# Kernel optimization log

Measured on AMD Instinct MI355X. Metric: run time of the kernel, lower is better.

## Reference

```python
import jax, jax.numpy as jnp
import numpy as np

D_MODEL = 1024
N_HEADS = 16
D_HEAD = D_MODEL // N_HEADS
SCALE = 1.0 / float(np.sqrt(D_HEAD))


def setup_inputs() -> dict:
    key = jax.random.key(0)
    ks = jax.random.split(key, 6)
    B, T = 4, 2048
    x = jax.random.normal(ks[0], (B, T, D_MODEL), dtype=jnp.float32)
    # torch Linear weights are [out, in]; y = x @ W.T
    s = 1.0 / np.sqrt(D_MODEL)
    Wq = jax.random.uniform(ks[1], (D_MODEL, D_MODEL), jnp.float32, -s, s)
    Wk = jax.random.uniform(ks[2], (D_MODEL, D_MODEL), jnp.float32, -s, s)
    Wv = jax.random.uniform(ks[3], (D_MODEL, D_MODEL), jnp.float32, -s, s)
    Wo = jax.random.uniform(ks[4], (D_MODEL, D_MODEL), jnp.float32, -s, s)
    bo = jax.random.uniform(ks[5], (D_MODEL,), jnp.float32, -s, s)
    return {"x": x, "Wq": Wq, "Wk": Wk, "Wv": Wv, "Wo": Wo, "bo": bo}


def reference(x, Wq, Wk, Wv, Wo, bo):
    B, T, D = x.shape
    # QKV projections (torch Linear: x @ W.T), split into heads -> [B, H, T, d]
    def heads(y):
        return y.reshape(B, T, N_HEADS, D_HEAD).transpose(0, 2, 1, 3)
    q = heads(x @ Wq.T)
    k = heads(x @ Wk.T)
    v = heads(x @ Wv.T)
    scores = jnp.einsum("bhqd,bhkd->bhqk", q, k) * SCALE  # [B,H,T,T]
    probs = jax.nn.softmax(scores, axis=-1)
    # dropout is identity in eval/inference mode
    out = jnp.einsum("bhqk,bhkd->bhqd", probs, v)  # [B,H,T,d]
    out = out.transpose(0, 2, 1, 3).reshape(B, T, D)
    return out @ Wo.T + bo
```

## Files before the change

### kernel.cpp

```cpp
#include <hip/hip_runtime.h>
#include <stdint.h>

#define D_MODEL 1024
#define NH 16
#define DH 64
#define TSEQ 2048
#define BATCH 4
#define MTOT (BATCH*TSEQ)
#define NQ (MTOT*D_MODEL)
#define WSZ (D_MODEL*D_MODEL)
#define QSCALE 0.18033688f

typedef __attribute__((ext_vector_type(8))) short bf16x8;
typedef __attribute__((ext_vector_type(8))) unsigned short u16x8;
typedef __attribute__((ext_vector_type(4))) float f32x4;
typedef __attribute__((ext_vector_type(2))) float f32x2;
typedef unsigned short u16;
typedef unsigned int u32;

__device__ __forceinline__ void gl_lds16(const void* g, void* l) {
  __builtin_amdgcn_global_load_lds(
      (__attribute__((address_space(1))) void*)g,
      (__attribute__((address_space(3))) void*)l, 16, 0, 0);
}
__device__ __forceinline__ u16 f2bf(float f) {
  u32 u = __builtin_bit_cast(u32, f);
  u = u + 0x7fffu + ((u >> 16) & 1u);
  return (u16)(u >> 16);
}
__device__ __forceinline__ float bf2f(u16 b) {
  u32 u = ((u32)b) << 16;
  return __builtin_bit_cast(float, u);
}
__device__ __forceinline__ u32 pack2bf(float fb, float fa) {
  const u32 ua = __builtin_bit_cast(u32, fa) + 0x8000u;
  const u32 ub = __builtin_bit_cast(u32, fb) + 0x8000u;
  return __builtin_amdgcn_perm(ua, ub, 0x07060302u);
}

__global__ __launch_bounds__(256) void detect_dtype(
    const u32* __restrict__ wq_raw, int* __restrict__ flag)
{
  __shared__ int cnt;
  if (threadIdx.x == 0) cnt = 0;
  __syncthreads();
  int c = 0;
  for (int i = threadIdx.x; i < 2048; i += 256) {
    const u32 e = (wq_raw[i] >> 7) & 0xFFu;
    if (e >= 90u && e <= 126u) ++c;
  }
  atomicAdd(&cnt, c);
  __syncthreads();
  if (threadIdx.x == 0) *flag = (cnt > 1024) ? 1 : 0;
}

__global__ __launch_bounds__(256) void convert_inputs(
    const void* __restrict__ x, const void* __restrict__ wq,
    const void* __restrict__ wk, const void* __restrict__ wv,
    const void* __restrict__ wo,
    u16* __restrict__ xb, u16* __restrict__ wqb, u16* __restrict__ wkb,
    u16* __restrict__ wvb, u16* __restrict__ wob,
    const int* __restrict__ flag_p)
{
  const int flag = *flag_p;
  const int seg = blockIdx.y;
  const void* src; u16* dst; int n;
  switch (seg) {
    case 0:  src = x;  dst = xb;  n = NQ;  break;
    case 1:  src = wq; dst = wqb; n = WSZ; break;
    case 2:  src = wk; dst = wkb; n = WSZ; break;
    case 3:  src = wv; dst = wvb; n = WSZ; break;
    default: src = wo; dst = wob; n = WSZ; break;
  }
  if (flag && seg == 0) return;
  const int idx = (blockIdx.x * 256 + threadIdx.x) * 8;
  if (idx >= n) return;
  if (flag) {
    *(u16x8*)(dst + idx) = *(const u16x8*)((const u16*)src + idx);
  } else {
    const float4 f0 = *(const float4*)((const float*)src + idx);
    const float4 f1 = *(const float4*)((const float*)src + idx + 4);
    union { u16 s[8]; u16x8 v; } u;
    u.s[0] = f2bf(f0.x); u.s[1] = f2bf(f0.y); u.s[2] = f2bf(f0.z); u.s[3] = f2bf(f0.w);
    u.s[4] = f2bf(f1.x); u.s[5] = f2bf(f1.y); u.s[6] = f2bf(f1.z); u.s[7] = f2bf(f1.w);
    *(u16x8*)(dst + idx) = u.v;
  }
}

__global__ __launch_bounds__(256) void qkv_gemm(
    const int* __restrict__ flag_p, const u16* __restrict__ x_raw,
    u16* __restrict__ dout,
    const u16* __restrict__ Wq, const u16* __restrict__ Wk,
    const u16* __restrict__ Wv,
    u16* __restrict__ Ko, u16* __restrict__ VTo)
{
  __shared__ __align__(16) u16 As[2 * 128 * 32];
  __shared__ __align__(16) u16 Bs[2 * 128 * 32];
  const int flag = *flag_p;
  const u16* __restrict__ X = flag ? x_raw : dout;
  u16* __restrict__ QTo = flag ? dout : dout + NQ;
  const int t = threadIdx.x;
  const int z = blockIdx.z;
  const u16* __restrict__ W = (z == 0) ? Wq : (z == 1) ? Wk : Wv;
  const int m0 = blockIdx.x * 128;
  const int n0 = blockIdx.y * 128;
  const int wave = t >> 6, lane = t & 63;
  const int wm = (wave >> 1) * 64, wn = (wave & 1) * 64;
  const int lr = lane & 15, kg = (lane >> 4) * 8;

  const int srow0 = t >> 2, skc = (t & 3) * 8;
  const int srow1 = srow0 + 64;
  const u16* a0 = X + (size_t)(m0 + srow0) * D_MODEL + skc;
  const u16* a1 = X + (size_t)(m0 + srow1) * D_MODEL + skc;
  const u16* b0 = W + (size_t)(n0 + srow0) * D_MODEL + skc;
  const u16* b1 = W + (size_t)(n0 + srow1) * D_MODEL + skc;

  f32x4 acc[4][4] = {};

  for (int kt = 0; kt < D_MODEL / 64; ++kt) {
    gl_lds16(a0,      &As[t * 8]);
    gl_lds16(a1,      &As[(t + 256) * 8]);
    gl_lds16(a0 + 32, &As[4096 + t * 8]);
    gl_lds16(a1 + 32, &As[4096 + (t + 256) * 8]);
    gl_lds16(b0,      &Bs[t * 8]);
    gl_lds16(b1,      &Bs[(t + 256) * 8]);
    gl_lds16(b0 + 32, &Bs[4096 + t * 8]);
    gl_lds16(b1 + 32, &Bs[4096 + (t + 256) * 8]);
    a0 += 64; a1 += 64; b0 += 64; b1 += 64;
    __syncthreads();
#pragma unroll
    for (int h = 0; h < 2; ++h) {
      bf16x8 af[4], bfr[4];
#pragma unroll
      for (int i = 0; i < 4; ++i)
        af[i] = *(const bf16x8*)&As[h * 4096 + (wm + i * 16 + lr) * 32 + kg];
#pragma unroll
      for (int j = 0; j < 4; ++j)
        bfr[j] = *(const bf16x8*)&Bs[h * 4096 + (wn + j * 16 + lr) * 32 + kg];
#pragma unroll
      for (int i = 0; i < 4; ++i)
#pragma unroll
        for (int j = 0; j < 4; ++j)
          acc[i][j] = __builtin_amdgcn_mfma_f32_16x16x32_bf16(af[i], bfr[j], acc[i][j], 0, 0, 0);
    }
    __syncthreads();
  }

  const int bidx = m0 >> 11;
  if (z == 1) {
#pragma unroll
    for (int i = 0; i < 4; ++i) {
      const int rowg = m0 + wm + i * 16 + ((lane >> 4) << 2);
      const int tq = rowg & (TSEQ - 1);
#pragma unroll
      for (int j = 0; j < 4; ++j) {
        const int colg = n0 + wn + j * 16 + lr;
        const int h = colg >> 6, d = colg & 63;
        u16* dst = Ko + ((size_t)(bidx * NH + h) * TSEQ + tq) * DH + d;
#pragma unroll
        for (int r = 0; r < 4; ++r)
          dst[(size_t)r * DH] = f2bf(acc[i][j][r]);
      }
    }
  } else {
    u16* O = (z == 0) ? QTo : VTo;
    const float sc = (z == 0) ? QSCALE : 1.0f;
#pragma unroll
    for (int i = 0; i < 4; ++i) {
      const int rowg = m0 + wm + i * 16 + ((lane >> 4) << 2);
      const int tq = rowg & (TSEQ - 1);
#pragma unroll
      for (int j = 0; j < 4; ++j) {
        const int colg = n0 + wn + j * 16 + lr;
        const int h = colg >> 6, d = colg & 63;
        union { u16 s[4]; uint2 v; } u;
#pragma unroll
        for (int r = 0; r < 4; ++r) u.s[r] = f2bf(acc[i][j][r] * sc);
        *(uint2*)&O[((size_t)(bidx * NH + h) * DH + d) * TSEQ + tq] = u.v;
      }
    }
  }
}

__global__ __launch_bounds__(256) void flash_attn(
    const int* __restrict__ flag_p, const u16* __restrict__ dout,
    const u16* __restrict__ K, const u16* __restrict__ VT,
    u16* __restrict__ AO)
{
  __shared__ __align__(16) u16 Ks[2 * 64 * 32];
  __shared__ __align__(16) u16 Vs[2 * 64 * 32];
  __shared__ __align__(16) u16 Ps[4 * 32 * 72];
  __shared__ float Ls[4 * 32];
  const int flag = *flag_p;
  const u16* __restrict__ QT = flag ? dout : dout + NQ;
  const int t = threadIdx.x;
  const int wave = t >> 6, lane = t & 63;
  const int lr = lane & 15, g = lane >> 4, kg = g * 8;
  const int bh = blockIdx.x;
  const int q0 = blockIdx.y * 128;
  const u16* __restrict__ QTh = QT + (size_t)bh * DH * TSEQ;
  const u16* __restrict__ Kh = K + (size_t)bh * TSEQ * DH;
  const u16* __restrict__ Vh = VT + (size_t)bh * DH * TSEQ;

  const int qiA = q0 + wave * 32 + lr;
  union { u16 s[8]; bf16x8 v; } qa0, qa1, qb0, qb1;
#pragma unroll
  for (int j = 0; j < 8; ++j) {
    qa0.s[j] = QTh[(size_t)(kg + j) * TSEQ + qiA];
    qa1.s[j] = QTh[(size_t)(32 + kg + j) * TSEQ + qiA];
    qb0.s[j] = QTh[(size_t)(kg + j) * TSEQ + qiA + 16];
    qb1.s[j] = QTh[(size_t)(32 + kg + j) * TSEQ + qiA + 16];
  }
  const bf16x8 qfA0 = qa0.v, qfA1 = qa1.v, qfB0 = qb0.v, qfB1 = qb1.v;

  f32x4 accA[4] = {}, accB[4] = {};
  f32x2 lsA0 = {0.f, 0.f}, lsA1 = {0.f, 0.f};
  f32x2 lsB0 = {0.f, 0.f}, lsB1 = {0.f, 0.f};

  const int srow = t >> 2, skc = (t & 3) * 8;
  const u16* kb = Kh + (size_t)srow * DH + skc;
  const u16* vb = Vh + (size_t)srow * TSEQ + skc;
  u16* const pw  = &Ps[wave * 32 * 72];
  u16* const pwB = pw + 16 * 72;

  for (int j0 = 0; j0 < TSEQ; j0 += 64) {
    gl_lds16(kb,      &Ks[t * 8]);
    gl_lds16(kb + 32, &Ks[(t + 256) * 8]);
    gl_lds16(vb,      &Vs[t * 8]);
    gl_lds16(vb + 32, &Vs[(t + 256) * 8]);
    kb += 64 * DH; vb += 64;
    __syncthreads();

#pragma unroll
    for (int jn = 0; jn < 4; ++jn) {
      const bf16x8 kf0 = *(const bf16x8*)&Ks[(jn * 16 + lr) * 32 + kg];
      const bf16x8 kf1 = *(const bf16x8*)&Ks[2048 + (jn * 16 + lr) * 32 + kg];
      f32x4 sA = {}, sB = {};
      sA = __builtin_amdgcn_mfma_f32_16x16x32_bf16(kf0, qfA0, sA, 0, 0, 0);
      sA = __builtin_amdgcn_mfma_f32_16x16x32_bf16(kf1, qfA1, sA, 0, 0, 0);
      sB = __builtin_amdgcn_mfma_f32_16x16x32_bf16(kf0, qfB0, sB, 0, 0, 0);
      sB = __builtin_amdgcn_mfma_f32_16x16x32_bf16(kf1, qfB1, sB, 0, 0, 0);
      const float a0 = __builtin_exp2f(sA[0]);
      const float a1 = __builtin_exp2f(sA[1]);
      const float a2 = __builtin_exp2f(sA[2]);
      const float a3 = __builtin_exp2f(sA[3]);
      const float b0 = __builtin_exp2f(sB[0]);
      const float b1 = __builtin_exp2f(sB[1]);
      const float b2 = __builtin_exp2f(sB[2]);
      const float b3 = __builtin_exp2f(sB[3]);
      lsA0 += (f32x2){a0, a1}; lsA1 += (f32x2){a2, a3};
      lsB0 += (f32x2){b0, b1}; lsB1 += (f32x2){b2, b3};
      uint2 wA, wB;
      wA.x = pack2bf(a0, a1); wA.y = pack2bf(a2, a3);
      wB.x = pack2bf(b0, b1); wB.y = pack2bf(b2, b3);
      *(uint2*)&pw [lr * 72 + jn * 16 + g * 4] = wA;
      *(uint2*)&pwB[lr * 72 + jn * 16 + g * 4] = wB;
    }

    const bf16x8 pfA0 = *(const bf16x8*)&pw [lr * 72 + kg];
    const bf16x8 pfA1 = *(const bf16x8*)&pw [lr * 72 + 32 + kg];
    const bf16x8 pfB0 = *(const bf16x8*)&pwB[lr * 72 + kg];
    const bf16x8 pfB1 = *(const bf16x8*)&pwB[lr * 72 + 32 + kg];
#pragma unroll
    for (int dn = 0; dn < 4; ++dn) {
      const bf16x8 vf0 = *(const bf16x8*)&Vs[(dn * 16 + lr) * 32 + kg];
      const bf16x8 vf1 = *(const bf16x8*)&Vs[2048 + (dn * 16 + lr) * 32 + kg];
      accA[dn] = __builtin_amdgcn_mfma_f32_16x16x32_bf16(pfA0, vf0, accA[dn], 0, 0, 0);
      accA[dn] = __builtin_amdgcn_mfma_f32_16x16x32_bf16(pfA1, vf1, accA[dn], 0, 0, 0);
      accB[dn] = __builtin_amdgcn_mfma_f32_16x16x32_bf16(pfB0, vf0, accB[dn], 0, 0, 0);
      accB[dn] = __builtin_amdgcn_mfma_f32_16x16x32_bf16(pfB1, vf1, accB[dn], 0, 0, 0);
    }
    __syncthreads();
  }

  float lA = (lsA0[0] + lsA0[1]) + (lsA1[0] + lsA1[1]);
  lA += __shfl_xor(lA, 16, 64);
  lA += __shfl_xor(lA, 32, 64);
  float lB = (lsB0[0] + lsB0[1]) + (lsB1[0] + lsB1[1]);
  lB += __shfl_xor(lB, 16, 64);
  lB += __shfl_xor(lB, 32, 64);
  Ls[wave * 32 + lr]      = lA;
  Ls[wave * 32 + 16 + lr] = lB;
  __syncthreads();

  const int bb = bh >> 4, hh = bh & 15;
#pragma unroll
  for (int r = 0; r < 4; ++r) {
    const int qq = g * 4 + r;
    const float invA = 1.f / fmaxf(Ls[wave * 32 + qq], 1e-30f);
    const float invB = 1.f / fmaxf(Ls[wave * 32 + 16 + qq], 1e-30f);
    const int tiA = q0 + wave * 32 + qq;
    u16* dstA = AO + (((size_t)bb * TSEQ + tiA) * NH + hh) * DH + lr;
    u16* dstB = AO + (((size_t)bb * TSEQ + tiA + 16) * NH + hh) * DH + lr;
#pragma unroll
    for (int dn = 0; dn < 4; ++dn) {
      dstA[dn * 16] = f2bf(accA[dn][r] * invA);
      dstB[dn * 16] = f2bf(accB[dn][r] * invB);
    }
  }
}

__global__ __launch_bounds__(256) void out_gemm(
    const int* __restrict__ flag_p,
    const u16* __restrict__ A, const u16* __restrict__ W,
    const void* __restrict__ bias_raw, void* __restrict__ outp)
{
  __shared__ __align__(16) u16 As[2 * 128 * 32];
  __shared__ __align__(16) u16 Bs[2 * 128 * 32];
  const int flag = *flag_p;
  const int t = threadIdx.x;
  const int m0 = blockIdx.x * 128;
  const int n0 = blockIdx.y * 128;
  const int wave = t >> 6, lane = t & 63;
  const int wm = (wave >> 1) * 64, wn = (wave & 1) * 64;
  const int lr = lane & 15, kg = (lane >> 4) * 8;

  const int srow0 = t >> 2, skc = (t & 3) * 8;
  const int srow1 = srow0 + 64;
  const u16* a0 = A + (size_t)(m0 + srow0) * D_MODEL + skc;
  const u16* a1 = A + (size_t)(m0 + srow1) * D_MODEL + skc;
  const u16* b0 = W + (size_t)(n0 + srow0) * D_MODEL + skc;
  const u16* b1 = W + (size_t)(n0 + srow1) * D_MODEL + skc;

  f32x4 acc[4][4] = {};

  for (int kt = 0; kt < D_MODEL / 64; ++kt) {
    gl_lds16(a0,      &As[t * 8]);
    gl_lds16(a1,      &As[(t + 256) * 8]);
    gl_lds16(a0 + 32, &As[4096 + t * 8]);
    gl_lds16(a1 + 32, &As[4096 + (t + 256) * 8]);
    gl_lds16(b0,      &Bs[t * 8]);
    gl_lds16(b1,      &Bs[(t + 256) * 8]);
    gl_lds16(b0 + 32, &Bs[4096 + t * 8]);
    gl_lds16(b1 + 32, &Bs[4096 + (t + 256) * 8]);
    a0 += 64; a1 += 64; b0 += 64; b1 += 64;
    __syncthreads();
#pragma unroll
    for (int h = 0; h < 2; ++h) {
      bf16x8 af[4], bfr[4];
#pragma unroll
      for (int i = 0; i < 4; ++i)
        af[i] = *(const bf16x8*)&As[h * 4096 + (wm + i * 16 + lr) * 32 + kg];
#pragma unroll
      for (int j = 0; j < 4; ++j)
        bfr[j] = *(const bf16x8*)&Bs[h * 4096 + (wn + j * 16 + lr) * 32 + kg];
#pragma unroll
      for (int i = 0; i < 4; ++i)
#pragma unroll
        for (int j = 0; j < 4; ++j)
          acc[i][j] = __builtin_amdgcn_mfma_f32_16x16x32_bf16(af[i], bfr[j], acc[i][j], 0, 0, 0);
    }
    __syncthreads();
  }

#pragma unroll
  for (int j = 0; j < 4; ++j) {
    const int colg = n0 + wn + j * 16 + lr;
    const float bv = flag ? bf2f(((const u16*)bias_raw)[colg])
                          : ((const float*)bias_raw)[colg];
#pragma unroll
    for (int i = 0; i < 4; ++i) {
      const int rowg = m0 + wm + i * 16 + ((lane >> 4) << 2);
      if (flag) {
        u16* dst = (u16*)outp + (size_t)rowg * D_MODEL + colg;
#pragma unroll
        for (int r = 0; r < 4; ++r)
          dst[(size_t)r * D_MODEL] = f2bf(acc[i][j][r] + bv);
      } else {
        float* dst = (float*)outp + (size_t)rowg * D_MODEL + colg;
#pragma unroll
        for (int r = 0; r < 4; ++r)
          dst[(size_t)r * D_MODEL] = acc[i][j][r] + bv;
      }
    }
  }
}

extern "C" void kernel_launch(void* const* d_in, const int* in_sizes, int n_in,
                              void* d_out, int out_size, void* d_ws, size_t ws_size,
                              hipStream_t stream) {
  const void* x  = d_in[0];
  const void* wq = d_in[1];
  const void* wk = d_in[2];
  const void* wv = d_in[3];
  const void* wo = d_in[4];
  const void* bo = d_in[5];
  u16* dout = (u16*)d_out;

  int* flag = (int*)d_ws;
  u16* wqb = (u16*)d_ws + 8;
  u16* wkb = wqb + WSZ;
  u16* wvb = wkb + WSZ;
  u16* wob = wvb + WSZ;
  u16* kk  = wob + WSZ;
  u16* vt  = kk + NQ;
  u16* ao  = vt + NQ;

  detect_dtype<<<1, 256, 0, stream>>>((const u32*)wq, flag);

  dim3 gc(NQ / (256 * 8), 5);
  convert_inputs<<<gc, dim3(256), 0, stream>>>(
      x, wq, wk, wv, wo, dout, wqb, wkb, wvb, wob, flag);

  dim3 g1(MTOT / 128, D_MODEL / 128, 3);
  qkv_gemm<<<g1, dim3(256), 0, stream>>>(
      flag, (const u16*)x, dout, wqb, wkb, wvb, kk, vt);

  dim3 g2(BATCH * NH, TSEQ / 128, 1);
  flash_attn<<<g2, dim3(256), 0, stream>>>(flag, dout, kk, vt, ao);

  dim3 g3(MTOT / 128, D_MODEL / 128, 1);
  out_gemm<<<g3, dim3(256), 0, stream>>>(flag, ao, wob, bo, d_out);
}
```

Baseline: 332.1 us.

## Double-buffer K/V tiles in flash attention and use hardware bf16 pack

K/V tiles in the attention loop now go into two LDS buffers. The next tile's global-to-LDS load is issued right after the barrier, so it overlaps with the MFMA and exp work on the current tile, and one barrier per iteration is dropped. Probability packing now uses the v_cvt_pk_bf16_f32 instruction instead of a manual add-and-permute sequence, which also changes rounding to round-to-nearest-even. The cost is doubled K/V LDS use, which could lower occupancy.

```diff
diff --git a/kernel.cpp b/kernel.cpp
--- a/kernel.cpp
+++ b/kernel.cpp
@@ -32,10 +32,10 @@
   u32 u = ((u32)b) << 16;
   return __builtin_bit_cast(float, u);
 }
-__device__ __forceinline__ u32 pack2bf(float fb, float fa) {
-  const u32 ua = __builtin_bit_cast(u32, fa) + 0x8000u;
-  const u32 ub = __builtin_bit_cast(u32, fb) + 0x8000u;
-  return __builtin_amdgcn_perm(ua, ub, 0x07060302u);
+__device__ __forceinline__ u32 cvtpk(float lo, float hi) {
+  u32 r;
+  asm("v_cvt_pk_bf16_f32 %0, %1, %2" : "=v"(r) : "v"(lo), "v"(hi));
+  return r;
 }
 
 __global__ __launch_bounds__(256) void detect_dtype(
@@ -187,8 +187,8 @@
     const u16* __restrict__ K, const u16* __restrict__ VT,
     u16* __restrict__ AO)
 {
-  __shared__ __align__(16) u16 Ks[2 * 64 * 32];
-  __shared__ __align__(16) u16 Vs[2 * 64 * 32];
+  __shared__ __align__(16) u16 Ks[2][2 * 64 * 32];
+  __shared__ __align__(16) u16 Vs[2][2 * 64 * 32];
   __shared__ __align__(16) u16 Ps[4 * 32 * 72];
   __shared__ float Ls[4 * 32];
   const int flag = *flag_p;
@@ -223,18 +223,29 @@
   u16* const pw  = &Ps[wave * 32 * 72];
   u16* const pwB = pw + 16 * 72;
 
+  gl_lds16(kb,      &Ks[0][t * 8]);
+  gl_lds16(kb + 32, &Ks[0][(t + 256) * 8]);
+  gl_lds16(vb,      &Vs[0][t * 8]);
+  gl_lds16(vb + 32, &Vs[0][(t + 256) * 8]);
+  kb += 64 * DH; vb += 64;
+
+  int cur = 0;
   for (int j0 = 0; j0 < TSEQ; j0 += 64) {
-    gl_lds16(kb,      &Ks[t * 8]);
-    gl_lds16(kb + 32, &Ks[(t + 256) * 8]);
-    gl_lds16(vb,      &Vs[t * 8]);
-    gl_lds16(vb + 32, &Vs[(t + 256) * 8]);
-    kb += 64 * DH; vb += 64;
     __syncthreads();
+    if (j0 + 64 < TSEQ) {
+      gl_lds16(kb,      &Ks[cur ^ 1][t * 8]);
+      gl_lds16(kb + 32, &Ks[cur ^ 1][(t + 256) * 8]);
+      gl_lds16(vb,      &Vs[cur ^ 1][t * 8]);
+      gl_lds16(vb + 32, &Vs[cur ^ 1][(t + 256) * 8]);
+      kb += 64 * DH; vb += 64;
+    }
+    const u16* __restrict__ Kc = Ks[cur];
+    const u16* __restrict__ Vc = Vs[cur];
 
 #pragma unroll
     for (int jn = 0; jn < 4; ++jn) {
-      const bf16x8 kf0 = *(const bf16x8*)&Ks[(jn * 16 + lr) * 32 + kg];
-      const bf16x8 kf1 = *(const bf16x8*)&Ks[2048 + (jn * 16 + lr) * 32 + kg];
+      const bf16x8 kf0 = *(const bf16x8*)&Kc[(jn * 16 + lr) * 32 + kg];
+      const bf16x8 kf1 = *(const bf16x8*)&Kc[2048 + (jn * 16 + lr) * 32 + kg];
       f32x4 sA = {}, sB = {};
       sA = __builtin_amdgcn_mfma_f32_16x16x32_bf16(kf0, qfA0, sA, 0, 0, 0);
       sA = __builtin_amdgcn_mfma_f32_16x16x32_bf16(kf1, qfA1, sA, 0, 0, 0);
@@ -251,8 +262,8 @@
       lsA0 += (f32x2){a0, a1}; lsA1 += (f32x2){a2, a3};
       lsB0 += (f32x2){b0, b1}; lsB1 += (f32x2){b2, b3};
       uint2 wA, wB;
-      wA.x = pack2bf(a0, a1); wA.y = pack2bf(a2, a3);
-      wB.x = pack2bf(b0, b1); wB.y = pack2bf(b2, b3);
+      wA.x = cvtpk(a0, a1); wA.y = cvtpk(a2, a3);
+      wB.x = cvtpk(b0, b1); wB.y = cvtpk(b2, b3);
       *(uint2*)&pw [lr * 72 + jn * 16 + g * 4] = wA;
       *(uint2*)&pwB[lr * 72 + jn * 16 + g * 4] = wB;
     }
@@ -263,14 +274,14 @@
     const bf16x8 pfB1 = *(const bf16x8*)&pwB[lr * 72 + 32 + kg];
 #pragma unroll
     for (int dn = 0; dn < 4; ++dn) {
-      const bf16x8 vf0 = *(const bf16x8*)&Vs[(dn * 16 + lr) * 32 + kg];
-      const bf16x8 vf1 = *(const bf16x8*)&Vs[2048 + (dn * 16 + lr) * 32 + kg];
+      const bf16x8 vf0 = *(const bf16x8*)&Vc[(dn * 16 + lr) * 32 + kg];
+      const bf16x8 vf1 = *(const bf16x8*)&Vc[2048 + (dn * 16 + lr) * 32 + kg];
       accA[dn] = __builtin_amdgcn_mfma_f32_16x16x32_bf16(pfA0, vf0, accA[dn], 0, 0, 0);
       accA[dn] = __builtin_amdgcn_mfma_f32_16x16x32_bf16(pfA1, vf1, accA[dn], 0, 0, 0);
       accB[dn] = __builtin_amdgcn_mfma_f32_16x16x32_bf16(pfB0, vf0, accB[dn], 0, 0, 0);
       accB[dn] = __builtin_amdgcn_mfma_f32_16x16x32_bf16(pfB1, vf1, accB[dn], 0, 0, 0);
     }
-    __syncthreads();
+    cur ^= 1;
   }
 
   float lA = (lsA0[0] + lsA0[1]) + (lsA1[0] + lsA1[1]);
```

After: 333.7 us. Within noise of the previous version (+0.5%).
